# Optimization experiments

Hardware: AMD Instinct MI355X
Metric: run time of the kernel (lower is better)

The kernel has to match this reference:

```python
import jax, jax.numpy as jnp
import numpy as np
import math

W = 256
H = 256
N = 1000
C = 1  # grayscale
ALPHA_MAX = 0.999


def _logit(p):
    return jnp.log(p) - jnp.log1p(-p)


def setup_inputs() -> dict:
    key = jax.random.key(0)
    k0, k1, k2, k3, k4 = jax.random.split(key, 5)
    means = jax.random.uniform(k0, (N, 2), dtype=jnp.float32) * W
    scales = jax.random.uniform(k1, (N, 2), dtype=jnp.float32) * 10.0 + 1.0
    quats = jax.random.uniform(k2, (N,), dtype=jnp.float32) * (2.0 * math.pi)  # rotation angle
    rgbs = _logit(jax.random.uniform(k3, (N, C), dtype=jnp.float32) * 0.3 + 0.1)
    opacities = _logit(jax.random.uniform(k4, (N,), dtype=jnp.float32) * 0.5 + 0.1)
    return {"means": means, "quats": quats, "scales": scales, "rgbs": rgbs, "opacities": opacities}


def _render(means, quats, scales, rgbs, opacities):
    # 2D covariance: Sigma = R diag(s^2) R^T, R = [[c,-s],[s,c]]
    c = jnp.cos(quats)
    s = jnp.sin(quats)
    sx2 = scales[:, 0] ** 2
    sy2 = scales[:, 1] ** 2
    a11 = c * c * sx2 + s * s * sy2
    a12 = c * s * (sx2 - sy2)
    a22 = s * s * sx2 + c * c * sy2
    det = a11 * a22 - a12 * a12
    ia = (a22 / det)[:, None, None]   # Sigma^-1 entries, broadcast over pixels
    ib = (-a12 / det)[:, None, None]
    ic = (a11 / det)[:, None, None]

    xs = jnp.arange(W, dtype=jnp.float32) + 0.5
    ys = jnp.arange(H, dtype=jnp.float32) + 0.5
    X = xs[None, :]   # [1, W] -> broadcasts to [H, W]
    Y = ys[:, None]   # [H, 1]

    dx = X[None] - means[:, 0, None, None]  # [N, H, W] (via broadcast)
    dy = Y[None] - means[:, 1, None, None]
    q = ia * dx * dx + 2.0 * ib * dx * dy + ic * dy * dy  # Mahalanobis^2, [N,H,W]

    opac = jax.nn.sigmoid(opacities)[:, None, None]
    alpha = jnp.minimum(opac * jnp.exp(-0.5 * q), ALPHA_MAX)  # [N,H,W]

    # Front-to-back compositing in index order: T_i = prod_{j<i} (1 - alpha_j)
    log_one_minus = jnp.log1p(-alpha)
    logT = jnp.cumsum(log_one_minus, axis=0) - log_one_minus  # exclusive cumsum
    weights = alpha * jnp.exp(logT)  # [N,H,W]

    colors = jax.nn.sigmoid(rgbs)  # [N,C]
    img = jnp.einsum('nhw,nc->chw', weights, colors)  # [C,H,W]
    return img[None]  # [1,C,H,W]


def reference(means, quats, scales, rgbs, opacities):
    return _render(means, quats, scales, rgbs, opacities)
```

## Files before the change

### kernel.cpp

```cpp
#include <hip/hip_runtime.h>
#include <math.h>

#define IW 256
#define IH 256
#define NG 1000
#define NSEG 4
#define SEG (NG / NSEG)
#define TILE_W 32
#define TILE_H 8
#define TILES_X (IW / TILE_W)
#define TILES_Y (IH / TILE_H)
#define ALPHA_MAX 0.999f
#define LOG2_EPS -19.93157f
#define LN2 0.6931471805599453f
#define INV_LN2 1.4426950408889634f

__global__ __launch_bounds__(256) void splat2d_segment_kernel(
    const float* __restrict__ means,
    const float* __restrict__ quats,
    const float* __restrict__ scales,
    const float* __restrict__ rgbs,
    const float* __restrict__ opacities,
    float2* __restrict__ segout)
{
    __shared__ float4 s0[SEG];
    __shared__ float4 s1[SEG];
    __shared__ int wave_cnt[4];
    __shared__ int s_count;

    const int tid = threadIdx.x;
    const int tx0 = blockIdx.x * TILE_W;
    const int ty0 = blockIdx.y * TILE_H;
    const int s   = blockIdx.z;
    const int n0g = s * SEG;

    const float midx = (float)tx0 + 0.5f * (TILE_W - 1) + 0.5f;
    const float midy = (float)ty0 + 0.5f * (TILE_H - 1) + 0.5f;
    const float hx = 0.5f * (TILE_W - 1);
    const float hy = 0.5f * (TILE_H - 1);

    bool keep = false;
    float cx, cy, A, B, Cc, lop, col;
    if (tid < SEG) {
        const int n = n0g + tid;
        float2 mu = ((const float2*)means)[n];
        float2 sc = ((const float2*)scales)[n];
        float q   = quats[n];
        float opa = opacities[n];
        float rgb = rgbs[n];

        float sq, cq;
        __sincosf(q, &sq, &cq);
        float sx2 = sc.x * sc.x, sy2 = sc.y * sc.y;
        float a11 = cq * cq * sx2 + sq * sq * sy2;
        float a12 = cq * sq * (sx2 - sy2);
        float a22 = sq * sq * sx2 + cq * cq * sy2;
        float det = a11 * a22 - a12 * a12;
        float inv = INV_LN2 / det;
        A   = -0.5f * a22 * inv;
        B   =          a12 * inv;
        Cc  = -0.5f * a11 * inv;
        float op = 1.0f / (1.0f + __expf(-opa));
        lop = __log2f(op);
        col = 1.0f / (1.0f + __expf(-rgb));
        cx = mu.x; cy = mu.y;

        float t  = fmaxf((lop - LOG2_EPS) * LN2, 0.0f);
        float rx = sqrtf(2.0f * a11 * t);
        float ry = sqrtf(2.0f * a22 * t);

        keep = (fabsf(cx - midx) <= hx + rx) &&
               (fabsf(cy - midy) <= hy + ry);
    }

    unsigned long long m = __ballot(keep);
    const int lane = tid & 63;
    const int w    = tid >> 6;
    int rank = __popcll(m & ((1ull << lane) - 1ull));
    if (lane == 0) wave_cnt[w] = __popcll(m);
    __syncthreads();
    int off = 0;
    #pragma unroll
    for (int i = 0; i < 4; ++i) if (i < w) off += wave_cnt[i];
    if (keep) {
        s0[off + rank] = make_float4(cx, cy, A, B);
        s1[off + rank] = make_float4(Cc, lop, col, 0.0f);
    }
    if (tid == 0) s_count = wave_cnt[0] + wave_cnt[1] + wave_cnt[2] + wave_cnt[3];
    __syncthreads();

    const float px = (float)(tx0 + (tid & (TILE_W - 1))) + 0.5f;
    const float py = (float)(ty0 + (tid >> 5)) + 0.5f;
    const int cnt = s_count;

    float T = 1.0f;
    float accum = 0.0f;

    for (int k = 0; k < cnt; ++k) {
        float4 q0 = s0[k];
        float4 q1 = s1[k];
        float dx = px - q0.x;
        float dy = py - q0.y;
        float t  = fmaf(q0.w, dy, q0.z * dx);
        float e  = fmaf(t, dx, fmaf(q1.x * dy, dy, q1.y));
        float alpha = fminf(__builtin_amdgcn_exp2f(e), ALPHA_MAX);
        accum = fmaf(alpha * T, q1.z, accum);
        T = fmaf(-alpha, T, T);
        if (((k & 7) == 7) && __all(T < 1e-5f)) break;
    }

    const int pix = (ty0 + (tid >> 5)) * IW + tx0 + (tid & (TILE_W - 1));
    segout[s * (IH * IW) + pix] = make_float2(accum, T);
}

__global__ __launch_bounds__(256) void splat2d_combine_kernel(
    const float2* __restrict__ segout,
    float* __restrict__ out)
{
    const int pix = blockIdx.x * 256 + threadIdx.x;

    float c = 0.0f;
    float T = 1.0f;
    #pragma unroll
    for (int s = 0; s < NSEG; ++s) {
        float2 v = segout[s * (IH * IW) + pix];
        c = fmaf(T, v.x, c);
        T *= v.y;
    }
    out[pix] = c;
}

extern "C" void kernel_launch(void* const* d_in, const int* in_sizes, int n_in,
                              void* d_out, int out_size, void* d_ws, size_t ws_size,
                              hipStream_t stream) {
    const float* means     = (const float*)d_in[0];
    const float* quats     = (const float*)d_in[1];
    const float* scales    = (const float*)d_in[2];
    const float* rgbs      = (const float*)d_in[3];
    const float* opacities = (const float*)d_in[4];
    float* out = (float*)d_out;

    float2* segout = (float2*)d_ws;

    splat2d_segment_kernel<<<dim3(TILES_X, TILES_Y, NSEG), 256, 0, stream>>>(
        means, quats, scales, rgbs, opacities, segout);
    splat2d_combine_kernel<<<(IH * IW) / 256, 256, 0, stream>>>(segout, out);
}
```

Measured before the change: 70.78 us.

## Fuse segment and combine kernels into single chunked per-tile compositing kernel

Result: slower. 77.82 us (+9.9%).

```diff
diff --git a/kernel.cpp b/kernel.cpp
--- a/kernel.cpp
+++ b/kernel.cpp
@@ -4,10 +4,9 @@
 #define IW 256
 #define IH 256
 #define NG 1000
-#define NSEG 4
-#define SEG (NG / NSEG)
-#define TILE_W 32
-#define TILE_H 8
+#define CHUNK 256
+#define TILE_W 16
+#define TILE_H 16
 #define TILES_X (IW / TILE_W)
 #define TILES_Y (IH / TILE_H)
 #define ALPHA_MAX 0.999f
@@ -15,119 +14,101 @@
 #define LN2 0.6931471805599453f
 #define INV_LN2 1.4426950408889634f
 
-__global__ __launch_bounds__(256) void splat2d_segment_kernel(
+__global__ __launch_bounds__(256) void splat2d_kernel(
     const float* __restrict__ means,
     const float* __restrict__ quats,
     const float* __restrict__ scales,
     const float* __restrict__ rgbs,
     const float* __restrict__ opacities,
-    float2* __restrict__ segout)
+    float* __restrict__ out)
 {
-    __shared__ float4 s0[SEG];
-    __shared__ float4 s1[SEG];
+    __shared__ float4 s0[CHUNK];
+    __shared__ float4 s1[CHUNK];
     __shared__ int wave_cnt[4];
-    __shared__ int s_count;
 
     const int tid = threadIdx.x;
     const int tx0 = blockIdx.x * TILE_W;
     const int ty0 = blockIdx.y * TILE_H;
-    const int s   = blockIdx.z;
-    const int n0g = s * SEG;
 
     const float midx = (float)tx0 + 0.5f * (TILE_W - 1) + 0.5f;
     const float midy = (float)ty0 + 0.5f * (TILE_H - 1) + 0.5f;
     const float hx = 0.5f * (TILE_W - 1);
     const float hy = 0.5f * (TILE_H - 1);
 
-    bool keep = false;
-    float cx, cy, A, B, Cc, lop, col;
-    if (tid < SEG) {
-        const int n = n0g + tid;
-        float2 mu = ((const float2*)means)[n];
-        float2 sc = ((const float2*)scales)[n];
-        float q   = quats[n];
-        float opa = opacities[n];
-        float rgb = rgbs[n];
+    const float px = (float)(tx0 + (tid & (TILE_W - 1))) + 0.5f;
+    const float py = (float)(ty0 + (tid >> 4)) + 0.5f;
 
-        float sq, cq;
-        __sincosf(q, &sq, &cq);
-        float sx2 = sc.x * sc.x, sy2 = sc.y * sc.y;
-        float a11 = cq * cq * sx2 + sq * sq * sy2;
-        float a12 = cq * sq * (sx2 - sy2);
-        float a22 = sq * sq * sx2 + cq * cq * sy2;
-        float det = a11 * a22 - a12 * a12;
-        float inv = INV_LN2 / det;
-        A   = -0.5f * a22 * inv;
-        B   =          a12 * inv;
-        Cc  = -0.5f * a11 * inv;
-        float op = 1.0f / (1.0f + __expf(-opa));
-        lop = __log2f(op);
-        col = 1.0f / (1.0f + __expf(-rgb));
-        cx = mu.x; cy = mu.y;
-
-        float t  = fmaxf((lop - LOG2_EPS) * LN2, 0.0f);
-        float rx = sqrtf(2.0f * a11 * t);
-        float ry = sqrtf(2.0f * a22 * t);
-
-        keep = (fabsf(cx - midx) <= hx + rx) &&
-               (fabsf(cy - midy) <= hy + ry);
-    }
-
-    unsigned long long m = __ballot(keep);
     const int lane = tid & 63;
     const int w    = tid >> 6;
-    int rank = __popcll(m & ((1ull << lane) - 1ull));
-    if (lane == 0) wave_cnt[w] = __popcll(m);
-    __syncthreads();
-    int off = 0;
-    #pragma unroll
-    for (int i = 0; i < 4; ++i) if (i < w) off += wave_cnt[i];
-    if (keep) {
-        s0[off + rank] = make_float4(cx, cy, A, B);
-        s1[off + rank] = make_float4(Cc, lop, col, 0.0f);
-    }
-    if (tid == 0) s_count = wave_cnt[0] + wave_cnt[1] + wave_cnt[2] + wave_cnt[3];
-    __syncthreads();
-
-    const float px = (float)(tx0 + (tid & (TILE_W - 1))) + 0.5f;
-    const float py = (float)(ty0 + (tid >> 5)) + 0.5f;
-    const int cnt = s_count;
 
     float T = 1.0f;
     float accum = 0.0f;
 
-    for (int k = 0; k < cnt; ++k) {
-        float4 q0 = s0[k];
-        float4 q1 = s1[k];
-        float dx = px - q0.x;
-        float dy = py - q0.y;
-        float t  = fmaf(q0.w, dy, q0.z * dx);
-        float e  = fmaf(t, dx, fmaf(q1.x * dy, dy, q1.y));
-        float alpha = fminf(__builtin_amdgcn_exp2f(e), ALPHA_MAX);
-        accum = fmaf(alpha * T, q1.z, accum);
-        T = fmaf(-alpha, T, T);
-        if (((k & 7) == 7) && __all(T < 1e-5f)) break;
+    for (int c0 = 0; c0 < NG; c0 += CHUNK) {
+        bool keep = false;
+        float cx, cy, A, B, Cc, lop, col;
+        const int n = c0 + tid;
+        if (n < NG) {
+            float2 mu = ((const float2*)means)[n];
+            float2 sc = ((const float2*)scales)[n];
+            float q   = quats[n];
+            float opa = opacities[n];
+            float rgb = rgbs[n];
+
+            float sq, cq;
+            __sincosf(q, &sq, &cq);
+            float sx2 = sc.x * sc.x, sy2 = sc.y * sc.y;
+            float a11 = cq * cq * sx2 + sq * sq * sy2;
+            float a12 = cq * sq * (sx2 - sy2);
+            float a22 = sq * sq * sx2 + cq * cq * sy2;
+            float det = a11 * a22 - a12 * a12;
+            float inv = INV_LN2 / det;
+            A   = -0.5f * a22 * inv;
+            B   =          a12 * inv;
+            Cc  = -0.5f * a11 * inv;
+            float op = 1.0f / (1.0f + __expf(-opa));
+            lop = __log2f(op);
+            col = 1.0f / (1.0f + __expf(-rgb));
+            cx = mu.x; cy = mu.y;
+
+            float t  = fmaxf((lop - LOG2_EPS) * LN2, 0.0f);
+            float rx = sqrtf(2.0f * a11 * t);
+            float ry = sqrtf(2.0f * a22 * t);
+
+            keep = (fabsf(cx - midx) <= hx + rx) &&
+                   (fabsf(cy - midy) <= hy + ry);
+        }
+
+        __syncthreads();
+        unsigned long long m = __ballot(keep);
+        int rank = __popcll(m & ((1ull << lane) - 1ull));
+        if (lane == 0) wave_cnt[w] = __popcll(m);
+        __syncthreads();
+        int c0w = wave_cnt[0], c1w = wave_cnt[1], c2w = wave_cnt[2], c3w = wave_cnt[3];
+        int off = (w > 0 ? c0w : 0) + (w > 1 ? c1w : 0) + (w > 2 ? c2w : 0);
+        const int cnt = c0w + c1w + c2w + c3w;
+        if (keep) {
+            s0[off + rank] = make_float4(cx, cy, A, B);
+            s1[off + rank] = make_float4(Cc, lop, col, 0.0f);
+        }
+        __syncthreads();
+
+        for (int k = 0; k < cnt; ++k) {
+            float4 q0 = s0[k];
+            float4 q1 = s1[k];
+            float dx = px - q0.x;
+            float dy = py - q0.y;
+            float t  = fmaf(q0.w, dy, q0.z * dx);
+            float e  = fmaf(t, dx, fmaf(q1.x * dy, dy, q1.y));
+            float alpha = fminf(__builtin_amdgcn_exp2f(e), ALPHA_MAX);
+            accum = fmaf(alpha * T, q1.z, accum);
+            T = fmaf(-alpha, T, T);
+            if (((k & 7) == 7) && __all(T < 1e-5f)) break;
+        }
     }
 
-    const int pix = (ty0 + (tid >> 5)) * IW + tx0 + (tid & (TILE_W - 1));
-    segout[s * (IH * IW) + pix] = make_float2(accum, T);
-}
-
-__global__ __launch_bounds__(256) void splat2d_combine_kernel(
-    const float2* __restrict__ segout,
-    float* __restrict__ out)
-{
-    const int pix = blockIdx.x * 256 + threadIdx.x;
-
-    float c = 0.0f;
-    float T = 1.0f;
-    #pragma unroll
-    for (int s = 0; s < NSEG; ++s) {
-        float2 v = segout[s * (IH * IW) + pix];
-        c = fmaf(T, v.x, c);
-        T *= v.y;
-    }
-    out[pix] = c;
+    const int pix = (ty0 + (tid >> 4)) * IW + tx0 + (tid & (TILE_W - 1));
+    out[pix] = accum;
 }
 
 extern "C" void kernel_launch(void* const* d_in, const int* in_sizes, int n_in,
@@ -140,9 +121,6 @@
     const float* opacities = (const float*)d_in[4];
     float* out = (float*)d_out;
 
-    float2* segout = (float2*)d_ws;
-
-    splat2d_segment_kernel<<<dim3(TILES_X, TILES_Y, NSEG), 256, 0, stream>>>(
-        means, quats, scales, rgbs, opacities, segout);
-    splat2d_combine_kernel<<<(IH * IW) / 256, 256, 0, stream>>>(segout, out);
+    splat2d_kernel<<<dim3(TILES_X, TILES_Y), 256, 0, stream>>>(
+        means, quats, scales, rgbs, opacities, out);
 }
```
